# Kernel tuning notes

Measured on AMD Instinct MI355X. Metric: run time of the kernel, lower is better.

## Reference

```python
import jax, jax.numpy as jnp
import numpy as np

N = 30000      # nodes
E = 480000     # edges (avg degree 16)
IN = 128       # atom in_channels
ED = 16        # edge_dim
D = 128        # hidden_channels
OUT = 64       # out_channels
L = 4          # num_layers + 1 GCNEConv layers


def setup_inputs() -> dict:
    key = jax.random.key(0)
    ks = jax.random.split(key, 8)
    w = lambda k, sh: (jax.random.normal(k, sh, dtype=jnp.float32) * 0.05)
    return {
        "x": jax.random.normal(ks[0], (N, IN), dtype=jnp.float32),
        "edge_index": jax.random.randint(ks[1], (2, E), 0, N, dtype=jnp.int64),
        "edge_attr": jax.random.normal(ks[2], (E, ED), dtype=jnp.float32),
        "W_atom": w(ks[3], (IN, D)), "b_atom": jnp.zeros((D,), jnp.float32),
        "W_bond": w(ks[4], (ED, D)), "b_bond": jnp.zeros((D,), jnp.float32),
        "W_seq": w(ks[5], (L, D, D)), "b_seq": jnp.zeros((L, D), jnp.float32),
        "W_lin": w(ks[6], (2 * D, OUT)), "b_lin": jnp.zeros((OUT,), jnp.float32),
    }


def _aggregate(h_bond, idx_i, n):
    # CMPNN 'message_booster': elementwise sum_agg * max_agg over incoming edges
    sum_agg = jax.ops.segment_sum(h_bond, idx_i, num_segments=n)
    max_agg = jax.ops.segment_max(h_bond, idx_i, num_segments=n)
    max_agg = jnp.where(jnp.isfinite(max_agg), max_agg, 0.0)  # empty segments -> 0
    return sum_agg * max_agg


def reference(x, edge_index, edge_attr, W_atom, b_atom, W_bond, b_bond,
              W_seq, b_seq, W_lin, b_lin):
    n = x.shape[0]
    idx_i = edge_index[0]  # flow='target_to_source' -> i is edge_index[0]
    idx_j = edge_index[1]

    x_proj = jax.nn.relu(x @ W_atom + b_atom)          # [N, D]
    h_atom = x_proj
    h_bond = jax.nn.relu(edge_attr @ W_bond + b_bond)  # [E, D]

    # first L-1 convs: node update + edge update
    for l in range(L - 1):
        msg = _aggregate(h_bond, idx_i, n)             # [N, D]
        h_atom = h_atom * msg                          # inner_product communicator
        # edge_update: x[edge_index_i] - edge_attr[edge_index_j] (node-index gather
        # into edge tensor, faithful to the original code; valid since E > N)
        bond = h_atom[idx_i] - h_bond[idx_j]           # [E, D]
        h_bond = jax.nn.relu(bond @ W_seq[l] + b_seq[l])

    # last conv: only the node output is used downstream
    msg = _aggregate(h_bond, idx_i, n)
    aggr_atom_message = h_atom * msg

    # top-level communicator (inner_product): hidden_state * message
    h_atom = h_atom * aggr_atom_message
    out = jnp.concatenate([h_atom, x_proj], axis=1) @ W_lin + b_lin  # [N, OUT]
    return out
```

## Files before the change

kernel.cpp:

```cpp
#include <hip/hip_runtime.h>
#include <hip/hip_bf16.h>

#define DD 128
#define SCB 256
#define CE  512

typedef __attribute__((ext_vector_type(8))) short bf16x8;
typedef __attribute__((ext_vector_type(4))) float f32x4;

__device__ __forceinline__ unsigned bf16_rne(float f) {
    unsigned u = __float_as_uint(f);
    return (u + 0x7fffu + ((u >> 16) & 1u)) >> 16;
}

__global__ __launch_bounds__(256)
void hist_kernel(const int* __restrict__ idx_i, int* __restrict__ cnt, int E)
{
    const int e = blockIdx.x * 256 + threadIdx.x;
    if (e < E) atomicAdd(&cnt[idx_i[e]], 1);
}

__global__ __launch_bounds__(SCB)
void scan1_kernel(const int* __restrict__ cnt, int* __restrict__ exc,
                  int* __restrict__ bsum, int n)
{
    __shared__ int s[SCB];
    const int i = blockIdx.x * SCB + (int)threadIdx.x;
    const int v = (i < n) ? cnt[i] : 0;
    s[threadIdx.x] = v;
    __syncthreads();
    #pragma unroll
    for (int off = 1; off < SCB; off <<= 1) {
        int t = (threadIdx.x >= off) ? s[threadIdx.x - off] : 0;
        __syncthreads();
        s[threadIdx.x] += t;
        __syncthreads();
    }
    if (i < n) exc[i] = s[threadIdx.x] - v;
    if (threadIdx.x == SCB - 1) bsum[blockIdx.x] = s[threadIdx.x];
}

__global__ __launch_bounds__(SCB)
void scan2_kernel(int* __restrict__ bsum, int nb)
{
    __shared__ int s[SCB];
    const int v = (threadIdx.x < nb) ? bsum[threadIdx.x] : 0;
    s[threadIdx.x] = v;
    __syncthreads();
    #pragma unroll
    for (int off = 1; off < SCB; off <<= 1) {
        int t = (threadIdx.x >= off) ? s[threadIdx.x - off] : 0;
        __syncthreads();
        s[threadIdx.x] += t;
        __syncthreads();
    }
    if (threadIdx.x < nb) bsum[threadIdx.x] = s[threadIdx.x] - v;
}

__global__ __launch_bounds__(SCB)
void scan3_kernel(int* __restrict__ exc, const int* __restrict__ bsum, int n)
{
    const int i = blockIdx.x * SCB + (int)threadIdx.x;
    if (i < n) exc[i] += bsum[i >> 8];
}

__global__ __launch_bounds__(256)
void scatter_kernel(const int* __restrict__ idx_i, const int* __restrict__ idx_j,
                    int* __restrict__ cursor, int* __restrict__ perm,
                    int* __restrict__ si, int* __restrict__ sj, int E)
{
    const int e = blockIdx.x * 256 + threadIdx.x;
    if (e < E) {
        const int n = idx_i[e];
        const int p = atomicAdd(&cursor[n], 1);
        perm[p] = e;
        si[p] = n;
        sj[p] = idx_j[e];
    }
}

__global__ __launch_bounds__(1024)
void gemm128_mfma_kernel(float* __restrict__ A0, const float* __restrict__ A1,
                         int nA, int nTotal,
                         const float* __restrict__ W, const float* __restrict__ bias,
                         int bias_limit, int do_relu, int update,
                         float* __restrict__ sum_agg, int* __restrict__ max_agg,
                         float* __restrict__ out0, float* __restrict__ out1,
                         int ntiles)
{
    __shared__ __align__(16) unsigned char SM[131584];
    char*  const Whi = (char*)SM;
    char*  const Wlo = (char*)SM + 32768;
    char*  const Ahi = (char*)SM + 65536;
    char*  const Alo = (char*)SM + 98304;
    float* const Wf  = (float*)(SM + 65536);
    float* const bs  = (float*)(SM + 131072);

    const int t = (int)threadIdx.x;

    {
        const float4* Wg = (const float4*)W;
        float4* Wd = (float4*)Wf;
        #pragma unroll
        for (int i = 0; i < 4; ++i) Wd[t + i * 1024] = Wg[t + i * 1024];
        if (t < DD) bs[t] = bias ? bias[t] : 0.f;
    }
    __syncthreads();
    {
        const int col = t >> 3;
        const int kb  = (t & 7) * 16;
        unsigned h16[16], l16[16];
        #pragma unroll
        for (int j = 0; j < 16; ++j) {
            const float w = Wf[(size_t)(kb + j) * DD + col];
            const unsigned hb = bf16_rne(w);
            const float hf = __uint_as_float(hb << 16);
            h16[j] = hb;
            l16[j] = bf16_rne(w - hf);
        }
        #pragma unroll
        for (int c = 0; c < 2; ++c) {
            uint4 ph, pl;
            ph.x = h16[c*8+0] | (h16[c*8+1] << 16);
            ph.y = h16[c*8+2] | (h16[c*8+3] << 16);
            ph.z = h16[c*8+4] | (h16[c*8+5] << 16);
            ph.w = h16[c*8+6] | (h16[c*8+7] << 16);
            pl.x = l16[c*8+0] | (l16[c*8+1] << 16);
            pl.y = l16[c*8+2] | (l16[c*8+3] << 16);
            pl.z = l16[c*8+4] | (l16[c*8+5] << 16);
            pl.w = l16[c*8+6] | (l16[c*8+7] << 16);
            const int off = ((col * 256 + (kb + c * 8) * 2)) ^ ((col & 7) << 4);
            *(uint4*)(Whi + off) = ph;
            *(uint4*)(Wlo + off) = pl;
        }
    }

    const int w  = t >> 6;
    const int l  = t & 63;
    const int wm = w >> 2;
    const int wn = w & 3;
    const int g  = l >> 4;
    const int q  = l & 15;

    for (int tile = blockIdx.x; tile < ntiles; tile += gridDim.x) {
        const int e0 = tile * 128;
        __syncthreads();

        #pragma unroll
        for (int i = 0; i < 2; ++i) {
            const int task = t + i * 1024;
            const int row  = task >> 4;
            const int c    = task & 15;
            const int rr = min(e0 + row, nTotal - 1);
            float d[8];
            if (rr < nA) {
                float* ph0 = A0 + (size_t)rr * DD + c * 8;
                const float4 a0 = *(const float4*)ph0;
                const float4 a1 = *(const float4*)(ph0 + 4);
                if (update) {
                    float* sp = sum_agg + (size_t)rr * DD + c * 8;
                    int*   mp = max_agg + (size_t)rr * DD + c * 8;
                    const float4 s0 = *(const float4*)sp;
                    const float4 s1 = *(const float4*)(sp + 4);
                    const int4   m0 = *(const int4*)mp;
                    const int4   m1 = *(const int4*)(mp + 4);
                    d[0] = a0.x * s0.x * __int_as_float(m0.x);
                    d[1] = a0.y * s0.y * __int_as_float(m0.y);
                    d[2] = a0.z * s0.z * __int_as_float(m0.z);
                    d[3] = a0.w * s0.w * __int_as_float(m0.w);
                    d[4] = a1.x * s1.x * __int_as_float(m1.x);
                    d[5] = a1.y * s1.y * __int_as_float(m1.y);
                    d[6] = a1.z * s1.z * __int_as_float(m1.z);
                    d[7] = a1.w * s1.w * __int_as_float(m1.w);
                    *(float4*)ph0       = make_float4(d[0], d[1], d[2], d[3]);
                    *(float4*)(ph0 + 4) = make_float4(d[4], d[5], d[6], d[7]);
                    *(float4*)sp       = make_float4(0.f, 0.f, 0.f, 0.f);
                    *(float4*)(sp + 4) = make_float4(0.f, 0.f, 0.f, 0.f);
                    *(int4*)mp       = make_int4(0, 0, 0, 0);
                    *(int4*)(mp + 4) = make_int4(0, 0, 0, 0);
                } else {
                    d[0] = a0.x; d[1] = a0.y; d[2] = a0.z; d[3] = a0.w;
                    d[4] = a1.x; d[5] = a1.y; d[6] = a1.z; d[7] = a1.w;
                }
            } else {
                const float* pa = A1 + (size_t)(rr - nA) * DD + c * 8;
                const float4 a0 = *(const float4*)pa;
                const float4 a1 = *(const float4*)(pa + 4);
                d[0] = a0.x; d[1] = a0.y; d[2] = a0.z; d[3] = a0.w;
                d[4] = a1.x; d[5] = a1.y; d[6] = a1.z; d[7] = a1.w;
            }
            unsigned h8[8], l8[8];
            #pragma unroll
            for (int j = 0; j < 8; ++j) {
                const unsigned hb = bf16_rne(d[j]);
                const float hf = __uint_as_float(hb << 16);
                h8[j] = hb;
                l8[j] = bf16_rne(d[j] - hf);
            }
            uint4 ph, pl;
            ph.x = h8[0] | (h8[1] << 16);
            ph.y = h8[2] | (h8[3] << 16);
            ph.z = h8[4] | (h8[5] << 16);
            ph.w = h8[6] | (h8[7] << 16);
            pl.x = l8[0] | (l8[1] << 16);
            pl.y = l8[2] | (l8[3] << 16);
            pl.z = l8[4] | (l8[5] << 16);
            pl.w = l8[6] | (l8[7] << 16);
            const int off = ((row * 256 + c * 16)) ^ ((row & 7) << 4);
            *(uint4*)(Ahi + off) = ph;
            *(uint4*)(Alo + off) = pl;
        }
        __syncthreads();

        f32x4 acc[2][2];
        const f32x4 zero = {0.f, 0.f, 0.f, 0.f};
        acc[0][0] = zero; acc[0][1] = zero; acc[1][0] = zero; acc[1][1] = zero;

        #pragma unroll
        for (int ks = 0; ks < 4; ++ks) {
            const int kbyte = ks * 64 + g * 16;
            bf16x8 ah[2], al[2], bh[2], bl[2];
            #pragma unroll
            for (int m = 0; m < 2; ++m) {
                const int row = wm * 32 + m * 16 + q;
                const int off = (row * 256 + kbyte) ^ ((row & 7) << 4);
                ah[m] = *(const bf16x8*)(Ahi + off);
                al[m] = *(const bf16x8*)(Alo + off);
            }
            #pragma unroll
            for (int n = 0; n < 2; ++n) {
                const int colv = wn * 32 + n * 16 + q;
                const int off = (colv * 256 + kbyte) ^ ((colv & 7) << 4);
                bh[n] = *(const bf16x8*)(Whi + off);
                bl[n] = *(const bf16x8*)(Wlo + off);
            }
            #pragma unroll
            for (int m = 0; m < 2; ++m)
                #pragma unroll
                for (int n = 0; n < 2; ++n)
                    acc[m][n] = __builtin_amdgcn_mfma_f32_16x16x32_bf16(ah[m], bh[n], acc[m][n], 0, 0, 0);
            #pragma unroll
            for (int m = 0; m < 2; ++m)
                #pragma unroll
                for (int n = 0; n < 2; ++n)
                    acc[m][n] = __builtin_amdgcn_mfma_f32_16x16x32_bf16(ah[m], bl[n], acc[m][n], 0, 0, 0);
            #pragma unroll
            for (int m = 0; m < 2; ++m)
                #pragma unroll
                for (int n = 0; n < 2; ++n)
                    acc[m][n] = __builtin_amdgcn_mfma_f32_16x16x32_bf16(al[m], bh[n], acc[m][n], 0, 0, 0);
        }

        #pragma unroll
        for (int n = 0; n < 2; ++n) {
            const int colv = wn * 32 + n * 16 + q;
            const float bv = bs[colv];
            #pragma unroll
            for (int m = 0; m < 2; ++m) {
                #pragma unroll
                for (int r = 0; r < 4; ++r) {
                    const int row = e0 + wm * 32 + m * 16 + g * 4 + r;
                    if (row < nTotal) {
                        float v = acc[m][n][r] + ((row < bias_limit) ? bv : 0.f);
                        if (do_relu) v = fmaxf(v, 0.f);
                        out0[(size_t)row * DD + colv] = v;
                        if (out1) out1[(size_t)row * DD + colv] = v;
                    }
                }
            }
        }
    }
}

__global__ __launch_bounds__(256)
void bond_proj_agg_kernel(const float* __restrict__ edge_attr,
                          const float* __restrict__ Wb, const float* __restrict__ bb,
                          const int* __restrict__ si, const int* __restrict__ perm,
                          float* __restrict__ h_head0,
                          float* __restrict__ sum_agg, int* __restrict__ max_agg,
                          int E, int N)
{
    __shared__ float Ws[16 * DD];
    __shared__ float bs2[DD];
    __shared__ __align__(16) float ea_s[32][16];
    __shared__ int ii2[32], pm2[32];

    for (int idx = (int)threadIdx.x; idx < 16 * DD; idx += 256) Ws[idx] = Wb[idx];
    if (threadIdx.x < DD) bs2[threadIdx.x] = bb[threadIdx.x];

    const int p0 = blockIdx.x * 32;
    {
        const int t = (int)threadIdx.x;
        const int row = t >> 3;
        const int k2 = (t & 7) * 2;
        const int ppc = min(p0 + row, E - 1);
        const int orig = perm[ppc];
        const float2 v2 = *(const float2*)(edge_attr + (size_t)orig * 16 + k2);
        ea_s[row][k2] = v2.x;
        ea_s[row][k2 + 1] = v2.y;
        if (t < 32) {
            const int q = min(p0 + t, E - 1);
            ii2[t] = si[q];
            pm2[t] = perm[q];
        }
    }
    __syncthreads();

    const int o    = threadIdx.x & 127;
    const int half = threadIdx.x >> 7;

    float wcol[16];
    #pragma unroll
    for (int k = 0; k < 16; ++k) wcol[k] = Ws[k * DD + o];
    const float bo = bs2[o];

    int curNode = ii2[half * 16];
    float rs = 0.f, rm = 0.f;
    #pragma unroll 4
    for (int j = 0; j < 16; ++j) {
        const int row = half * 16 + j;
        const float4* ear = (const float4*)(&ea_s[row][0]);
        const float4 q0 = ear[0], q1 = ear[1], q2 = ear[2], q3 = ear[3];
        float acc = bo;
        acc = fmaf(q0.x, wcol[ 0], acc);
        acc = fmaf(q0.y, wcol[ 1], acc);
        acc = fmaf(q0.z, wcol[ 2], acc);
        acc = fmaf(q0.w, wcol[ 3], acc);
        acc = fmaf(q1.x, wcol[ 4], acc);
        acc = fmaf(q1.y, wcol[ 5], acc);
        acc = fmaf(q1.z, wcol[ 6], acc);
        acc = fmaf(q1.w, wcol[ 7], acc);
        acc = fmaf(q2.x, wcol[ 8], acc);
        acc = fmaf(q2.y, wcol[ 9], acc);
        acc = fmaf(q2.z, wcol[10], acc);
        acc = fmaf(q2.w, wcol[11], acc);
        acc = fmaf(q3.x, wcol[12], acc);
        acc = fmaf(q3.y, wcol[13], acc);
        acc = fmaf(q3.z, wcol[14], acc);
        acc = fmaf(q3.w, wcol[15], acc);
        float v = fmaxf(acc, 0.f);
        const int pe = p0 + row;
        if (pe < E) {
            const int orig = pm2[row];
            if (orig < N) h_head0[(size_t)orig * DD + o] = v;
        } else {
            v = 0.f;
        }
        const int gi = ii2[row];
        if (gi != curNode) {
            atomicAdd(&sum_agg[(size_t)curNode * DD + o], rs);
            atomicMax(&max_agg[(size_t)curNode * DD + o], __float_as_int(rm));
            curNode = gi; rs = v; rm = v;
        } else {
            rs += v; rm = fmaxf(rm, v);
        }
    }
    atomicAdd(&sum_agg[(size_t)curNode * DD + o], rs);
    atomicMax(&max_agg[(size_t)curNode * DD + o], __float_as_int(rm));
}

__global__ __launch_bounds__(256)
void edge_pass_kernel(const float* __restrict__ PQ,
                      const int* __restrict__ si, const int* __restrict__ sj,
                      const int* __restrict__ perm,
                      float* __restrict__ head_next, int store_head,
                      float* __restrict__ sum_agg, int* __restrict__ max_agg,
                      int E, int N)
{
    __shared__ int si_s[CE], sj_s[CE], pm_s[CE];
    const int p0b = blockIdx.x * CE;
    if (p0b >= E) return;
    const int t = (int)threadIdx.x;
    for (int i = t; i < CE; i += 256) {
        const int p = min(p0b + i, E - 1);
        si_s[i] = si[p];
        sj_s[i] = sj[p];
        pm_s[i] = perm[p];
    }
    __syncthreads();

    const int w    = t >> 6;
    const int lane = t & 63;
    const int c    = lane * 2;
    const int q0   = w * 128;
    const int pg0  = p0b + q0;
    if (pg0 >= E) return;

    const int firstNode = si_s[q0];
    const int lastNode  = si_s[q0 + 127];

    const float* __restrict__ Qbase = PQ + (size_t)N * DD + c;

    float2 qa = *(const float2*)(Qbase + (size_t)sj_s[q0 + 0] * DD);
    float2 qb = *(const float2*)(Qbase + (size_t)sj_s[q0 + 1] * DD);
    float2 qc = *(const float2*)(Qbase + (size_t)sj_s[q0 + 2] * DD);
    float2 qd = *(const float2*)(Qbase + (size_t)sj_s[q0 + 3] * DD);

    int curNode = firstNode;
    float2 Pi = *(const float2*)(PQ + (size_t)curNode * DD + c);
    float2 rs = make_float2(0.f, 0.f), rm = make_float2(0.f, 0.f);

    #define EP_FLUSH()                                                           \
    {                                                                            \
        if (curNode == firstNode || curNode == lastNode) {                       \
            atomicAdd(&sum_agg[(size_t)curNode * DD + c],     rs.x);             \
            atomicAdd(&sum_agg[(size_t)curNode * DD + c + 1], rs.y);             \
            atomicMax(&max_agg[(size_t)curNode * DD + c],     __float_as_int(rm.x)); \
            atomicMax(&max_agg[(size_t)curNode * DD + c + 1], __float_as_int(rm.y)); \
        } else {                                                                 \
            *(float2*)(sum_agg + (size_t)curNode * DD + c) = rs;                 \
            *(int2*)(max_agg + (size_t)curNode * DD + c) =                       \
                make_int2(__float_as_int(rm.x), __float_as_int(rm.y));           \
        }                                                                        \
    }

    #define EP_STEP(K, QREG)                                                     \
    {                                                                            \
        const int kk = (K);                                                      \
        const int i = si_s[q0 + kk];                                             \
        if (i != curNode) {                                                      \
            EP_FLUSH();                                                          \
            curNode = i;                                                         \
            Pi = *(const float2*)(PQ + (size_t)i * DD + c);                      \
            rs = make_float2(0.f, 0.f);                                          \
            rm = make_float2(0.f, 0.f);                                          \
        }                                                                        \
        float2 v;                                                                \
        v.x = fmaxf(Pi.x - QREG.x, 0.f);                                         \
        v.y = fmaxf(Pi.y - QREG.y, 0.f);                                         \
        if (pg0 + kk >= E) { v.x = 0.f; v.y = 0.f; }                             \
        rs.x += v.x; rs.y += v.y;                                                \
        rm.x = fmaxf(rm.x, v.x); rm.y = fmaxf(rm.y, v.y);                        \
        if (store_head && (pg0 + kk) < E) {                                      \
            const int orig = pm_s[q0 + kk];                                      \
            if (orig < N) *(float2*)(head_next + (size_t)orig * DD + c) = v;     \
        }                                                                        \
        if (kk + 4 < 128)                                                        \
            QREG = *(const float2*)(Qbase + (size_t)sj_s[q0 + kk + 4] * DD);     \
    }

    #pragma unroll 8
    for (int k = 0; k < 128; k += 4) {
        EP_STEP(k + 0, qa);
        EP_STEP(k + 1, qb);
        EP_STEP(k + 2, qc);
        EP_STEP(k + 3, qd);
    }
    EP_FLUSH();
    #undef EP_STEP
    #undef EP_FLUSH
}

__global__ __launch_bounds__(512, 2)
void final_mfma_kernel(const float* __restrict__ h, const float* __restrict__ sum_agg,
                       const int* __restrict__ max_agg, const float* __restrict__ xp,
                       const float* __restrict__ Wl, const float* __restrict__ bl,
                       float* __restrict__ out, int N)
{
    __shared__ __align__(16) unsigned char SM[65808];
    char*  const Whi = (char*)SM;
    char*  const Wlo = (char*)SM + 32768;
    float* const Wf  = (float*)SM;
    float* const bs  = (float*)(SM + 65536);

    const int t = (int)threadIdx.x;
    {
        const float4* Wg = (const float4*)Wl;
        float4* Wd = (float4*)Wf;
        #pragma unroll
        for (int i = 0; i < 8; ++i) Wd[t + i * 512] = Wg[t + i * 512];
        if (t < 64) bs[t] = bl[t];
    }
    __syncthreads();
    {
        const int col = t & 63;
        const int kb  = (t >> 6) * 32;
        float v[32];
        #pragma unroll
        for (int j = 0; j < 32; ++j) v[j] = Wf[(size_t)(kb + j) * 64 + col];
        __syncthreads();
        #pragma unroll
        for (int c = 0; c < 4; ++c) {
            unsigned h8[8], l8[8];
            #pragma unroll
            for (int j = 0; j < 8; ++j) {
                const float w0 = v[c * 8 + j];
                const unsigned hb = bf16_rne(w0);
                h8[j] = hb;
                l8[j] = bf16_rne(w0 - __uint_as_float(hb << 16));
            }
            uint4 ph, pl;
            ph.x = h8[0] | (h8[1] << 16); ph.y = h8[2] | (h8[3] << 16);
            ph.z = h8[4] | (h8[5] << 16); ph.w = h8[6] | (h8[7] << 16);
            pl.x = l8[0] | (l8[1] << 16); pl.y = l8[2] | (l8[3] << 16);
            pl.z = l8[4] | (l8[5] << 16); pl.w = l8[6] | (l8[7] << 16);
            const int off = (col * 512 + (kb + c * 8) * 2) ^ ((col & 7) << 4);
            *(uint4*)(Whi + off) = ph;
            *(uint4*)(Wlo + off) = pl;
        }
    }
    __syncthreads();

    const int w  = t >> 6;
    const int l  = t & 63;
    const int wm = w >> 1;
    const int wn = w & 1;
    const int g  = l >> 4;
    const int q  = l & 15;
    const int r0 = (int)blockIdx.x * 128;

    f32x4 acc[2][2];
    const f32x4 zero = {0.f, 0.f, 0.f, 0.f};
    acc[0][0] = zero; acc[0][1] = zero; acc[1][0] = zero; acc[1][1] = zero;

    #pragma unroll
    for (int ks = 0; ks < 8; ++ks) {
        const int kf = (ks & 3) * 32 + g * 8;
        bf16x8 ah[2], al[2];
        #pragma unroll
        for (int m = 0; m < 2; ++m) {
            const int rr = min(r0 + wm * 32 + m * 16 + q, N - 1);
            float d[8];
            if (ks < 4) {
                const float* ph = h       + (size_t)rr * DD + kf;
                const float* ps = sum_agg + (size_t)rr * DD + kf;
                const int*   pm = max_agg + (size_t)rr * DD + kf;
                const float4 a0 = *(const float4*)ph;
                const float4 a1 = *(const float4*)(ph + 4);
                const float4 s0 = *(const float4*)ps;
                const float4 s1 = *(const float4*)(ps + 4);
                const int4   i0 = *(const int4*)pm;
                const int4   i1 = *(const int4*)(pm + 4);
                d[0] = a0.x * a0.x * s0.x * __int_as_float(i0.x);
                d[1] = a0.y * a0.y * s0.y * __int_as_float(i0.y);
                d[2] = a0.z * a0.z * s0.z * __int_as_float(i0.z);
                d[3] = a0.w * a0.w * s0.w * __int_as_float(i0.w);
                d[4] = a1.x * a1.x * s1.x * __int_as_float(i1.x);
                d[5] = a1.y * a1.y * s1.y * __int_as_float(i1.y);
                d[6] = a1.z * a1.z * s1.z * __int_as_float(i1.z);
                d[7] = a1.w * a1.w * s1.w * __int_as_float(i1.w);
            } else {
                const float* pa = xp + (size_t)rr * DD + kf;
                const float4 a0 = *(const float4*)pa;
                const float4 a1 = *(const float4*)(pa + 4);
                d[0] = a0.x; d[1] = a0.y; d[2] = a0.z; d[3] = a0.w;
                d[4] = a1.x; d[5] = a1.y; d[6] = a1.z; d[7] = a1.w;
            }
            unsigned h8[8], l8[8];
            #pragma unroll
            for (int j = 0; j < 8; ++j) {
                const unsigned hb = bf16_rne(d[j]);
                h8[j] = hb;
                l8[j] = bf16_rne(d[j] - __uint_as_float(hb << 16));
            }
            uint4 ph2, pl2;
            ph2.x = h8[0] | (h8[1] << 16); ph2.y = h8[2] | (h8[3] << 16);
            ph2.z = h8[4] | (h8[5] << 16); ph2.w = h8[6] | (h8[7] << 16);
            pl2.x = l8[0] | (l8[1] << 16); pl2.y = l8[2] | (l8[3] << 16);
            pl2.z = l8[4] | (l8[5] << 16); pl2.w = l8[6] | (l8[7] << 16);
            ah[m] = *(bf16x8*)&ph2;
            al[m] = *(bf16x8*)&pl2;
        }
        bf16x8 bh[2], blo[2];
        #pragma unroll
        for (int n = 0; n < 2; ++n) {
            const int colv = wn * 32 + n * 16 + q;
            const int off = (colv * 512 + ks * 64 + g * 16) ^ ((colv & 7) << 4);
            bh[n]  = *(const bf16x8*)(Whi + off);
            blo[n] = *(const bf16x8*)(Wlo + off);
        }
        #pragma unroll
        for (int m = 0; m < 2; ++m)
            #pragma unroll
            for (int n = 0; n < 2; ++n) {
                acc[m][n] = __builtin_amdgcn_mfma_f32_16x16x32_bf16(ah[m], bh[n],  acc[m][n], 0, 0, 0);
                acc[m][n] = __builtin_amdgcn_mfma_f32_16x16x32_bf16(ah[m], blo[n], acc[m][n], 0, 0, 0);
                acc[m][n] = __builtin_amdgcn_mfma_f32_16x16x32_bf16(al[m], bh[n],  acc[m][n], 0, 0, 0);
            }
    }

    #pragma unroll
    for (int n = 0; n < 2; ++n) {
        const int colv = wn * 32 + n * 16 + q;
        const float bv = bs[colv];
        #pragma unroll
        for (int m = 0; m < 2; ++m) {
            #pragma unroll
            for (int r = 0; r < 4; ++r) {
                const int row = r0 + wm * 32 + m * 16 + g * 4 + r;
                if (row < N) out[(size_t)row * 64 + colv] = acc[m][n][r] + bv;
            }
        }
    }
}

extern "C" void kernel_launch(void* const* d_in, const int* in_sizes, int n_in,
                              void* d_out, int out_size, void* d_ws, size_t ws_size,
                              hipStream_t stream)
{
    const float* x         = (const float*)d_in[0];
    const int*   edge_idx  = (const int*)d_in[1];
    const float* edge_attr = (const float*)d_in[2];
    const float* W_atom    = (const float*)d_in[3];
    const float* b_atom    = (const float*)d_in[4];
    const float* W_bond    = (const float*)d_in[5];
    const float* b_bond    = (const float*)d_in[6];
    const float* W_seq     = (const float*)d_in[7];
    const float* b_seq     = (const float*)d_in[8];
    const float* W_lin     = (const float*)d_in[9];
    const float* b_lin     = (const float*)d_in[10];
    float* out = (float*)d_out;

    const int N = in_sizes[0] / DD;
    const int E = in_sizes[1] / 2;
    const int* idx_i = edge_idx;
    const int* idx_j = edge_idx + E;

    const size_t nd = (size_t)N * DD;
    float* ws      = (float*)d_ws;
    float* x_proj  = ws;
    float* h_atom  = x_proj + nd;
    float* head    = h_atom + nd;
    float* sum_agg = head + nd;
    int*   max_agg = (int*)(sum_agg + nd);
    float* PQ      = (float*)(max_agg + nd);
    int*   cnt     = (int*)(PQ + 2 * nd);
    int*   cursor  = cnt + N;
    int*   bsum    = cursor + N;
    int*   perm    = bsum + 256;
    int*   si      = perm + E;
    int*   sj      = si + E;

    hipMemsetAsync(cnt, 0, (size_t)N * 4, stream);
    hist_kernel<<<(E + 255) / 256, 256, 0, stream>>>(idx_i, cnt, E);
    const int nb_scan = (N + SCB - 1) / SCB;
    scan1_kernel<<<nb_scan, SCB, 0, stream>>>(cnt, cursor, bsum, N);
    scan2_kernel<<<1, SCB, 0, stream>>>(bsum, nb_scan);
    scan3_kernel<<<nb_scan, SCB, 0, stream>>>(cursor, bsum, N);
    scatter_kernel<<<(E + 255) / 256, 256, 0, stream>>>(idx_i, idx_j, cursor, perm, si, sj, E);

    hipMemsetAsync(sum_agg, 0, nd * 4, stream);
    hipMemsetAsync(max_agg, 0, nd * 4, stream);

    const int ntiles_n = (N + 127) / 128;
    gemm128_mfma_kernel<<<min(ntiles_n, 256), 1024, 0, stream>>>(
        (float*)x, x, N, N, W_atom, b_atom, N, 1, 0, nullptr, nullptr,
        x_proj, h_atom, ntiles_n);

    bond_proj_agg_kernel<<<(E + 31) / 32, 256, 0, stream>>>(edge_attr, W_bond, b_bond,
                                                            si, perm, head,
                                                            sum_agg, max_agg, E, N);

    const int ntiles_pq = (2 * N + 127) / 128;
    const int ep_blocks = (E + CE - 1) / CE;
    for (int l = 0; l < 3; ++l) {
        gemm128_mfma_kernel<<<256, 1024, 0, stream>>>(
            h_atom, head, N, 2 * N, W_seq + (size_t)l * DD * DD,
            b_seq + (size_t)l * DD, N, 0, 1, sum_agg, max_agg,
            PQ, nullptr, ntiles_pq);
        edge_pass_kernel<<<ep_blocks, 256, 0, stream>>>(
            PQ, si, sj, perm, head, (l < 2) ? 1 : 0, sum_agg, max_agg, E, N);
    }

    final_mfma_kernel<<<(N + 127) / 128, 512, 0, stream>>>(
        h_atom, sum_agg, (const int*)max_agg, x_proj, W_lin, b_lin, out, N);
}
```

Measured before the change: 440.1 us.

## Restructure bond projection pass: per-wave 128-edge runs with plain stores for interior nodes

```diff
diff --git a/kernel.cpp b/kernel.cpp
--- a/kernel.cpp
+++ b/kernel.cpp
@@ -4,6 +4,7 @@
 #define DD 128
 #define SCB 256
 #define CE  512
+#define CB  512
 
 typedef __attribute__((ext_vector_type(8))) short bf16x8;
 typedef __attribute__((ext_vector_type(4))) float f32x4;
@@ -273,90 +274,111 @@
 }
 
 __global__ __launch_bounds__(256)
-void bond_proj_agg_kernel(const float* __restrict__ edge_attr,
-                          const float* __restrict__ Wb, const float* __restrict__ bb,
-                          const int* __restrict__ si, const int* __restrict__ perm,
-                          float* __restrict__ h_head0,
-                          float* __restrict__ sum_agg, int* __restrict__ max_agg,
-                          int E, int N)
-{
-    __shared__ float Ws[16 * DD];
-    __shared__ float bs2[DD];
-    __shared__ __align__(16) float ea_s[32][16];
-    __shared__ int ii2[32], pm2[32];
-
-    for (int idx = (int)threadIdx.x; idx < 16 * DD; idx += 256) Ws[idx] = Wb[idx];
-    if (threadIdx.x < DD) bs2[threadIdx.x] = bb[threadIdx.x];
-
-    const int p0 = blockIdx.x * 32;
-    {
-        const int t = (int)threadIdx.x;
-        const int row = t >> 3;
-        const int k2 = (t & 7) * 2;
-        const int ppc = min(p0 + row, E - 1);
-        const int orig = perm[ppc];
-        const float2 v2 = *(const float2*)(edge_attr + (size_t)orig * 16 + k2);
-        ea_s[row][k2] = v2.x;
-        ea_s[row][k2 + 1] = v2.y;
-        if (t < 32) {
-            const int q = min(p0 + t, E - 1);
-            ii2[t] = si[q];
-            pm2[t] = perm[q];
-        }
+void bond_pass_kernel(const float* __restrict__ edge_attr,
+                      const float* __restrict__ Wb, const float* __restrict__ bb,
+                      const int* __restrict__ si, const int* __restrict__ perm,
+                      float* __restrict__ h_head0,
+                      float* __restrict__ sum_agg, int* __restrict__ max_agg,
+                      int E, int N)
+{
+    __shared__ __align__(16) float ea_s[CB][16];
+    __shared__ int si_s[CB], pm_s[CB];
+
+    const int p0b = blockIdx.x * CB;
+    if (p0b >= E) return;
+    const int t = (int)threadIdx.x;
+
+    for (int i = t; i < CB; i += 256) {
+        const int p = min(p0b + i, E - 1);
+        si_s[i] = si[p];
+        pm_s[i] = perm[p];
+    }
+    for (int task = t; task < CB * 4; task += 256) {
+        const int row = task >> 2;
+        const int c4  = task & 3;
+        const int p = min(p0b + row, E - 1);
+        const int orig = perm[p];
+        *(float4*)(&ea_s[row][c4 * 4]) =
+            *(const float4*)(edge_attr + (size_t)orig * 16 + c4 * 4);
     }
     __syncthreads();
 
-    const int o    = threadIdx.x & 127;
-    const int half = threadIdx.x >> 7;
-
-    float wcol[16];
+    const int w    = t >> 6;
+    const int lane = t & 63;
+    const int c    = lane * 2;
+    const int q0   = w * 128;
+    const int pg0  = p0b + q0;
+    if (pg0 >= E) return;
+
+    float wc0[16], wc1[16];
     #pragma unroll
-    for (int k = 0; k < 16; ++k) wcol[k] = Ws[k * DD + o];
-    const float bo = bs2[o];
-
-    int curNode = ii2[half * 16];
-    float rs = 0.f, rm = 0.f;
+    for (int k = 0; k < 16; ++k) {
+        const float2 wv = *(const float2*)(Wb + k * DD + c);
+        wc0[k] = wv.x; wc1[k] = wv.y;
+    }
+    const float2 bc = *(const float2*)(bb + c);
+
+    const int firstNode = si_s[q0];
+    const int lastNode  = si_s[q0 + 127];
+
+    int curNode = firstNode;
+    float2 rs = make_float2(0.f, 0.f), rm = make_float2(0.f, 0.f);
+
+    #define BP_FLUSH()                                                           \
+    {                                                                            \
+        if (curNode == firstNode || curNode == lastNode) {                       \
+            atomicAdd(&sum_agg[(size_t)curNode * DD + c],     rs.x);             \
+            atomicAdd(&sum_agg[(size_t)curNode * DD + c + 1], rs.y);             \
+            atomicMax(&max_agg[(size_t)curNode * DD + c],     __float_as_int(rm.x)); \
+            atomicMax(&max_agg[(size_t)curNode * DD + c + 1], __float_as_int(rm.y)); \
+        } else {                                                                 \
+            *(float2*)(sum_agg + (size_t)curNode * DD + c) = rs;                 \
+            *(int2*)(max_agg + (size_t)curNode * DD + c) =                       \
+                make_int2(__float_as_int(rm.x), __float_as_int(rm.y));           \
+        }                                                                        \
+    }
+
     #pragma unroll 4
-    for (int j = 0; j < 16; ++j) {
-        const int row = half * 16 + j;
-        const float4* ear = (const float4*)(&ea_s[row][0]);
-        const float4 q0 = ear[0], q1 = ear[1], q2 = ear[2], q3 = ear[3];
-        float acc = bo;
-        acc = fmaf(q0.x, wcol[ 0], acc);
-        acc = fmaf(q0.y, wcol[ 1], acc);
-        acc = fmaf(q0.z, wcol[ 2], acc);
-        acc = fmaf(q0.w, wcol[ 3], acc);
-        acc = fmaf(q1.x, wcol[ 4], acc);
-        acc = fmaf(q1.y, wcol[ 5], acc);
-        acc = fmaf(q1.z, wcol[ 6], acc);
-        acc = fmaf(q1.w, wcol[ 7], acc);
-        acc = fmaf(q2.x, wcol[ 8], acc);
-        acc = fmaf(q2.y, wcol[ 9], acc);
-        acc = fmaf(q2.z, wcol[10], acc);
-        acc = fmaf(q2.w, wcol[11], acc);
-        acc = fmaf(q3.x, wcol[12], acc);
-        acc = fmaf(q3.y, wcol[13], acc);
-        acc = fmaf(q3.z, wcol[14], acc);
-        acc = fmaf(q3.w, wcol[15], acc);
-        float v = fmaxf(acc, 0.f);
-        const int pe = p0 + row;
-        if (pe < E) {
-            const int orig = pm2[row];
-            if (orig < N) h_head0[(size_t)orig * DD + o] = v;
-        } else {
-            v = 0.f;
-        }
-        const int gi = ii2[row];
-        if (gi != curNode) {
-            atomicAdd(&sum_agg[(size_t)curNode * DD + o], rs);
-            atomicMax(&max_agg[(size_t)curNode * DD + o], __float_as_int(rm));
-            curNode = gi; rs = v; rm = v;
-        } else {
-            rs += v; rm = fmaxf(rm, v);
-        }
-    }
-    atomicAdd(&sum_agg[(size_t)curNode * DD + o], rs);
-    atomicMax(&max_agg[(size_t)curNode * DD + o], __float_as_int(rm));
+    for (int kk = 0; kk < 128; ++kk) {
+        const int i = si_s[q0 + kk];
+        if (i != curNode) {
+            BP_FLUSH();
+            curNode = i;
+            rs = make_float2(0.f, 0.f);
+            rm = make_float2(0.f, 0.f);
+        }
+        const float4* ear = (const float4*)(&ea_s[q0 + kk][0]);
+        const float4 e0 = ear[0], e1 = ear[1], e2 = ear[2], e3 = ear[3];
+        float ax = bc.x, ay = bc.y;
+        ax = fmaf(e0.x, wc0[ 0], ax);  ay = fmaf(e0.x, wc1[ 0], ay);
+        ax = fmaf(e0.y, wc0[ 1], ax);  ay = fmaf(e0.y, wc1[ 1], ay);
+        ax = fmaf(e0.z, wc0[ 2], ax);  ay = fmaf(e0.z, wc1[ 2], ay);
+        ax = fmaf(e0.w, wc0[ 3], ax);  ay = fmaf(e0.w, wc1[ 3], ay);
+        ax = fmaf(e1.x, wc0[ 4], ax);  ay = fmaf(e1.x, wc1[ 4], ay);
+        ax = fmaf(e1.y, wc0[ 5], ax);  ay = fmaf(e1.y, wc1[ 5], ay);
+        ax = fmaf(e1.z, wc0[ 6], ax);  ay = fmaf(e1.z, wc1[ 6], ay);
+        ax = fmaf(e1.w, wc0[ 7], ax);  ay = fmaf(e1.w, wc1[ 7], ay);
+        ax = fmaf(e2.x, wc0[ 8], ax);  ay = fmaf(e2.x, wc1[ 8], ay);
+        ax = fmaf(e2.y, wc0[ 9], ax);  ay = fmaf(e2.y, wc1[ 9], ay);
+        ax = fmaf(e2.z, wc0[10], ax);  ay = fmaf(e2.z, wc1[10], ay);
+        ax = fmaf(e2.w, wc0[11], ax);  ay = fmaf(e2.w, wc1[11], ay);
+        ax = fmaf(e3.x, wc0[12], ax);  ay = fmaf(e3.x, wc1[12], ay);
+        ax = fmaf(e3.y, wc0[13], ax);  ay = fmaf(e3.y, wc1[13], ay);
+        ax = fmaf(e3.z, wc0[14], ax);  ay = fmaf(e3.z, wc1[14], ay);
+        ax = fmaf(e3.w, wc0[15], ax);  ay = fmaf(e3.w, wc1[15], ay);
+        float2 v;
+        v.x = fmaxf(ax, 0.f);
+        v.y = fmaxf(ay, 0.f);
+        if (pg0 + kk >= E) { v.x = 0.f; v.y = 0.f; }
+        rs.x += v.x; rs.y += v.y;
+        rm.x = fmaxf(rm.x, v.x); rm.y = fmaxf(rm.y, v.y);
+        if (pg0 + kk < E) {
+            const int orig = pm_s[q0 + kk];
+            if (orig < N) *(float2*)(h_head0 + (size_t)orig * DD + c) = v;
+        }
+    }
+    BP_FLUSH();
+    #undef BP_FLUSH
 }
 
 __global__ __launch_bounds__(256)
@@ -647,9 +669,8 @@
         (float*)x, x, N, N, W_atom, b_atom, N, 1, 0, nullptr, nullptr,
         x_proj, h_atom, ntiles_n);
 
-    bond_proj_agg_kernel<<<(E + 31) / 32, 256, 0, stream>>>(edge_attr, W_bond, b_bond,
-                                                            si, perm, head,
-                                                            sum_agg, max_agg, E, N);
+    bond_pass_kernel<<<(E + CB - 1) / CB, 256, 0, stream>>>(
+        edge_attr, W_bond, b_bond, si, perm, head, sum_agg, max_agg, E, N);
 
     const int ntiles_pq = (2 * N + 127) / 128;
     const int ep_blocks = (E + CE - 1) / CE;
```

Measured after the change: 429.8 us. 2.3% less time.
